# Kernel tuning notes

Hardware: AMD Instinct MI355X
Metric: run time of the kernel (lower is better)

## Reference

```python
import jax, jax.numpy as jnp
import numpy as np

S1, S2 = 1024, 1024
DA, DV, DOUT = 2, 64, 1
K1, K2 = 32, 32


def _gelu(x):
    # torch nn.GELU() default is the exact erf-based gelu
    return jax.nn.gelu(x, approximate=False)


def _flayer(Rr, Ri, w, x):
    f = jnp.fft.rfftn(x, axes=(0, 1))[:K1, :K2]            # [K1,K2,DV] complex
    Rf = jnp.einsum('abc,abcd->abd', f, Rr + 1j * Ri)       # [K1,K2,DV] complex
    kernelpart = jnp.fft.irfftn(Rf, s=(S1, S2), axes=(0, 1))  # [S1,S2,DV] real
    return _gelu(kernelpart + x @ w)


def setup_inputs() -> dict:
    key = jax.random.key(0)
    ks = jax.random.split(key, 20)
    d = {}
    d['input'] = jax.random.normal(ks[0], (S1, S2, DA), dtype=jnp.float32)
    d['Wsh'] = jax.random.normal(ks[1], (DA, DV), dtype=jnp.float32) * (1.0 / np.sqrt(DA))
    d['bsh'] = jax.random.normal(ks[2], (DV,), dtype=jnp.float32) * 0.02
    for i, base in zip(range(1, 5), range(3, 15, 3)):
        d[f'Rr{i}'] = jax.random.normal(ks[base], (K1, K2, DV, DV), dtype=jnp.float32) * (1.0 / DV)
        d[f'Ri{i}'] = jax.random.normal(ks[base + 1], (K1, K2, DV, DV), dtype=jnp.float32) * (1.0 / DV)
        d[f'w{i}'] = jax.random.normal(ks[base + 2], (DV, DV), dtype=jnp.float32) * (1.0 / np.sqrt(DV))
    d['Wp'] = jax.random.normal(ks[15], (DV, DOUT), dtype=jnp.float32) * (1.0 / np.sqrt(DV))
    d['bp'] = jax.random.normal(ks[16], (DOUT,), dtype=jnp.float32) * 0.02
    return d


def reference(input, Wsh, bsh, Rr1, Ri1, w1, Rr2, Ri2, w2,
              Rr3, Ri3, w3, Rr4, Ri4, w4, Wp, bp):
    vt = _gelu(input @ Wsh + bsh)          # Shallow: Linear + GELU
    vt = _flayer(Rr1, Ri1, w1, vt)
    vt = _flayer(Rr2, Ri2, w2, vt)
    vt = _flayer(Rr3, Ri3, w3, vt)
    vt = _flayer(Rr4, Ri4, w4, vt)
    u = (vt @ Wp + bp)[:, :, 0]            # Project, take channel 0 -> [S1,S2]
    return u
```

## Files before the change

### kernel.cpp

```cpp
#include <hip/hip_runtime.h>
#include <math.h>

#define MASKN 1023

typedef unsigned short ushort_t;
typedef __attribute__((ext_vector_type(8))) short short8;
typedef __attribute__((ext_vector_type(4))) float floatx4;
typedef __attribute__((ext_vector_type(4))) unsigned short us4v;

__device__ __forceinline__ float gelu_f(float x) {
    float x2 = x * x;
    float inner = fmaf(0.044715f * x, x2, x);
    float t = exp2f(inner * -2.302089214f);
    return x * __builtin_amdgcn_rcpf(1.0f + t);
}

__device__ __forceinline__ float bf2f(ushort_t h) {
    return __uint_as_float(((unsigned int)h) << 16);
}
__device__ __forceinline__ ushort_t f2bf(float f) {
    unsigned int u = __float_as_uint(f);
    u += 0x7FFFu + ((u >> 16) & 1u);
    return (ushort_t)(u >> 16);
}
struct us4 { ushort_t x, y, z, w; };

__device__ __forceinline__ unsigned int pk2bf(float lo, float hi) {
    unsigned int r;
    asm("v_cvt_pk_bf16_f32 %0, %1, %2" : "=v"(r) : "v"(lo), "v"(hi));
    return r;
}

__device__ __forceinline__ void st4(ushort_t* p, float4 v) {
    uint2 w;
    w.x = pk2bf(v.x, v.y);
    w.y = pk2bf(v.z, v.w);
    *(uint2*)p = w;
}

__device__ __forceinline__ void async16(ushort_t* l, const ushort_t* g) {
    __builtin_amdgcn_global_load_lds(
        (const __attribute__((address_space(1))) void*)g,
        (__attribute__((address_space(3))) void*)l, 16, 0, 0);
}

__global__ void k_fill_tw(float* __restrict__ ct, float* __restrict__ st) {
    int j = blockIdx.x * 256 + threadIdx.x;
    float ang = (float)j * (6.283185307179586f / 1024.0f);
    float s, c;
    sincosf(ang, &s, &c);
    ct[j] = c; st[j] = s;
}

__global__ void k_fill_T1(ushort_t* __restrict__ T1h, ushort_t* __restrict__ T1l) {
    int idx = blockIdx.x * 256 + threadIdx.x;
    int k2p = idx >> 10, y = idx & 1023;
    int k2 = k2p >> 1;
    float ang = (float)((k2 * y) & MASKN) * (6.283185307179586f / 1024.0f);
    float s, c;
    sincosf(ang, &s, &c);
    float v = (k2p & 1) ? -s : c;
    ushort_t h = f2bf(v);
    T1h[idx] = h;
    T1l[idx] = f2bf(v - bf2f(h));
}

__global__ void k_fill_T2(ushort_t* __restrict__ T2h, ushort_t* __restrict__ T2l) {
    int idx = blockIdx.x * 256 + threadIdx.x;
    int n2 = idx >> 6, kk = idx & 63;
    int k2 = kk >> 1;
    float ang = (float)((k2 * n2) & MASKN) * (6.283185307179586f / 1024.0f);
    float s, c;
    sincosf(ang, &s, &c);
    float v = (kk & 1) ? -s : c;
    ushort_t h = f2bf(v);
    T2h[idx] = h;
    T2l[idx] = f2bf(v - bf2f(h));
}

__global__ void k_fill_wT(const float* __restrict__ w1, const float* __restrict__ w2,
        const float* __restrict__ w3, const float* __restrict__ w4,
        ushort_t* __restrict__ wTh, ushort_t* __restrict__ wTl) {
    int l = blockIdx.y;
    int i = blockIdx.x * 256 + threadIdx.x;
    int d = i >> 6, c = i & 63;
    const float* w = (l == 0) ? w1 : (l == 1) ? w2 : (l == 2) ? w3 : w4;
    float v = w[c * 64 + d];
    ushort_t h = f2bf(v);
    wTh[l * 4096 + i] = h;
    wTl[l * 4096 + i] = f2bf(v - bf2f(h));
}

__global__ __launch_bounds__(256) void k_shallow(const float* __restrict__ in,
        const float* __restrict__ Wsh, const float* __restrict__ bsh,
        ushort_t* __restrict__ vt) {
    int tid = blockIdx.x * 256 + threadIdx.x;
    int p = tid >> 4, c0 = (tid & 15) << 2;
    float a0 = in[p * 2], a1 = in[p * 2 + 1];
    float4 w0 = *(const float4*)&Wsh[c0];
    float4 w1 = *(const float4*)&Wsh[64 + c0];
    float4 b  = *(const float4*)&bsh[c0];
    float4 r;
    r.x = gelu_f(fmaf(a0, w0.x, fmaf(a1, w1.x, b.x)));
    r.y = gelu_f(fmaf(a0, w0.y, fmaf(a1, w1.y, b.y)));
    r.z = gelu_f(fmaf(a0, w0.z, fmaf(a1, w1.z, b.z)));
    r.w = gelu_f(fmaf(a0, w0.w, fmaf(a1, w1.w, b.w)));
    st4(&vt[(size_t)p * 64 + c0], r);
}

#define VS1 72
__global__ __launch_bounds__(256, 3) void k_f1(const ushort_t* __restrict__ vt,
        const ushort_t* __restrict__ T1h, const ushort_t* __restrict__ T1l,
        float* __restrict__ gT) {
    __shared__ __align__(16) ushort_t t1s[2][8192];
    __shared__ __align__(16) ushort_t vs[2][64 * VS1];
    int t = threadIdx.x;
    int x0 = blockIdx.x * 2;
    int wv = t >> 6, lane = t & 63;
    int lm = lane & 15, quad = lane >> 4;
    int lrow = t & 63, cq = (t >> 6) * 16;
    const ushort_t* vrow0 = vt + (size_t)x0 * 65536;
    const ushort_t* vrow1 = vrow0 + 65536;

    floatx4 acc[2][4];
    #pragma unroll
    for (int xi = 0; xi < 2; ++xi)
        #pragma unroll
        for (int nt = 0; nt < 4; ++nt) acc[xi][nt] = (floatx4)(0.f);

    uint4 pf[2][2][2];
    #pragma unroll
    for (int i = 0; i < 4; ++i) {
        int j = (wv * 4 + i) * 64 + lane;
        int jj = j & 511;
        int r = jj >> 3, du = jj & 7, su = du ^ (r & 7);
        const ushort_t* src = ((j < 512) ? T1h : T1l) + (size_t)r * 1024 + su * 8;
        async16(&t1s[0][(wv * 4 + i) * 512], src);
    }
    __builtin_amdgcn_sched_barrier(0);
    {
        const ushort_t* s00 = vrow0 + (size_t)lrow * 64 + cq;
        pf[0][0][0] = *(const uint4*)(s00);
        pf[0][0][1] = *(const uint4*)(s00 + 8);
        const ushort_t* s01 = vrow1 + (size_t)lrow * 64 + cq;
        pf[0][1][0] = *(const uint4*)(s01);
        pf[0][1][1] = *(const uint4*)(s01 + 8);
        const ushort_t* s10 = vrow0 + (size_t)(64 + lrow) * 64 + cq;
        pf[1][0][0] = *(const uint4*)(s10);
        pf[1][0][1] = *(const uint4*)(s10 + 8);
        const ushort_t* s11 = vrow1 + (size_t)(64 + lrow) * 64 + cq;
        pf[1][1][0] = *(const uint4*)(s11);
        pf[1][1][1] = *(const uint4*)(s11 + 8);
    }
    __builtin_amdgcn_sched_barrier(0);

    for (int hc = 0; hc < 16; ++hc) {
        int b = hc & 1;
        #pragma unroll
        for (int xi = 0; xi < 2; ++xi)
            #pragma unroll
            for (int i = 0; i < 2; ++i) {
                union { uint4 u; ushort_t e[8]; } uv;
                uv.u = pf[b][xi][i];
                #pragma unroll
                for (int j = 0; j < 8; ++j)
                    vs[xi][(cq + i * 8 + j) * VS1 + lrow] = uv.e[j];
            }
        __builtin_amdgcn_sched_barrier(0);
        if (hc < 15) asm volatile("s_waitcnt vmcnt(4)" ::: "memory");
        else         asm volatile("s_waitcnt vmcnt(0)" ::: "memory");
        __builtin_amdgcn_sched_barrier(0);
        __builtin_amdgcn_s_barrier();
        if (hc < 15) {
            #pragma unroll
            for (int i = 0; i < 4; ++i) {
                int j = (wv * 4 + i) * 64 + lane;
                int jj = j & 511;
                int r = jj >> 3, du = jj & 7, su = du ^ (r & 7);
                const ushort_t* src = ((j < 512) ? T1h : T1l)
                                      + (size_t)r * 1024 + (hc + 1) * 64 + su * 8;
                async16(&t1s[b ^ 1][(wv * 4 + i) * 512], src);
            }
        }
        if (hc < 14) {
            const ushort_t* s0 = vrow0 + (size_t)((hc + 2) * 64 + lrow) * 64 + cq;
            pf[b][0][0] = *(const uint4*)(s0);
            pf[b][0][1] = *(const uint4*)(s0 + 8);
            const ushort_t* s1 = vrow1 + (size_t)((hc + 2) * 64 + lrow) * 64 + cq;
            pf[b][1][0] = *(const uint4*)(s1);
            pf[b][1][1] = *(const uint4*)(s1 + 8);
        }
        __builtin_amdgcn_sched_barrier(0);

        #pragma unroll
        for (int ys = 0; ys < 2; ++ys) {
            short8 af0 = *(const short8*)&vs[0][(wv * 16 + lm) * VS1 + ys * 32 + quad * 8];
            short8 af1 = *(const short8*)&vs[1][(wv * 16 + lm) * VS1 + ys * 32 + quad * 8];
            #pragma unroll
            for (int nt = 0; nt < 4; ++nt) {
                int sl = (((ys * 4 + quad) ^ (lm & 7)) * 8);
                short8 bh = *(const short8*)&t1s[b][(nt * 16 + lm) * 64 + sl];
                short8 bl = *(const short8*)&t1s[b][4096 + (nt * 16 + lm) * 64 + sl];
                acc[0][nt] = __builtin_amdgcn_mfma_f32_16x16x32_bf16(af0, bh, acc[0][nt], 0, 0, 0);
                acc[0][nt] = __builtin_amdgcn_mfma_f32_16x16x32_bf16(af0, bl, acc[0][nt], 0, 0, 0);
                acc[1][nt] = __builtin_amdgcn_mfma_f32_16x16x32_bf16(af1, bh, acc[1][nt], 0, 0, 0);
                acc[1][nt] = __builtin_amdgcn_mfma_f32_16x16x32_bf16(af1, bl, acc[1][nt], 0, 0, 0);
            }
        }
    }
    #pragma unroll
    for (int xi = 0; xi < 2; ++xi) {
        float* grow = gT + (size_t)(x0 + xi) * 4096;
        #pragma unroll
        for (int nt = 0; nt < 4; ++nt)
            #pragma unroll
            for (int r = 0; r < 4; ++r)
                grow[(wv * 16 + quad * 4 + r) * 64 + nt * 16 + lm] = acc[xi][nt][r];
    }
}

__global__ __launch_bounds__(256) void k_f2(const float* __restrict__ gT,
        const float* __restrict__ ct, const float* __restrict__ st,
        float* __restrict__ fpr, float* __restrict__ fpi) {
    int t = threadIdx.x;
    int cx = blockIdx.x;
    int cg = blockIdx.y;
    int k10 = blockIdx.z * 8;
    int l = t & 63;
    int q = t >> 6;
    int c = cg * 4 + q;
    int e = l & 1;
    int k2 = l >> 1;
    float acc[8];
    #pragma unroll
    for (int i = 0; i < 8; ++i) acc[i] = 0.f;
    for (int xi = 0; xi < 128; ++xi) {
        int x = cx * 128 + xi;
        float v = gT[(size_t)x * 4096 + c * 64 + l];
        float p = __shfl_xor(v, 1);
        float gr = e ? p : v;
        float gi = e ? v : p;
        float u  = e ? gi : gr;
        float w2 = e ? -gr : gi;
        float cb = ct[x], sb = st[x];
        int ph = (x * k10) & MASKN;
        float cr = ct[ph], sr = st[ph];
        #pragma unroll
        for (int j = 0; j < 8; ++j) {
            acc[j] = fmaf(u, cr, fmaf(w2, sr, acc[j]));
            float nc = fmaf(cr, cb, -sr * sb);
            float ns = fmaf(sr, cb, cr * sb);
            cr = nc; sr = ns;
        }
    }
    float* dst = e ? fpi : fpr;
    #pragma unroll
    for (int j = 0; j < 8; ++j)
        dst[(size_t)cx * 65536 + ((k10 + j) * 32 + k2) * 64 + c] = acc[j];
}

__global__ __launch_bounds__(64) void k_mix(const float* __restrict__ fpr, const float* __restrict__ fpi,
        const float* __restrict__ Rr, const float* __restrict__ Ri,
        float* __restrict__ Rfr, float* __restrict__ Rfi) {
    __shared__ float fr[64], fi[64];
    int m = blockIdx.x;
    int d = threadIdx.x;
    float sr = 0.f, si = 0.f;
    #pragma unroll
    for (int ch = 0; ch < 8; ++ch) {
        sr += fpr[(size_t)ch * 65536 + m * 64 + d];
        si += fpi[(size_t)ch * 65536 + m * 64 + d];
    }
    fr[d] = sr; fi[d] = si;
    __syncthreads();
    const float* Rrb = Rr + (size_t)m * 4096;
    const float* Rib = Ri + (size_t)m * 4096;
    float ar = 0.f, ai = 0.f;
    for (int c = 0; c < 64; ++c) {
        float rr = Rrb[c * 64 + d], ri = Rib[c * 64 + d];
        ar = fmaf(fr[c], rr, fmaf(-fi[c], ri, ar));
        ai = fmaf(fr[c], ri, fmaf(fi[c], rr, ai));
    }
    Rfr[m * 64 + d] = ar;
    Rfi[m * 64 + d] = ai;
}

__global__ __launch_bounds__(256) void k_i1(const float* __restrict__ Rfr, const float* __restrict__ Rfi,
        const float* __restrict__ ctg, const float* __restrict__ stg,
        ushort_t* __restrict__ Bhl) {
    __shared__ float ct[1024], st[1024];
    int t = threadIdx.x;
    #pragma unroll
    for (int i = 0; i < 4; ++i) { int j = t + 256 * i; ct[j] = ctg[j]; st[j] = stg[j]; }
    __syncthreads();
    int n1 = blockIdx.x;
    int d = t & 63;
    int k20 = (t >> 6) * 8;
    float br[8], bi[8];
    #pragma unroll
    for (int j = 0; j < 8; ++j) { br[j] = 0.f; bi[j] = 0.f; }
    int idx = 0;
    for (int k1 = 0; k1 < 32; ++k1) {
        float cc = ct[idx], ss = st[idx];
        idx = (idx + n1) & MASKN;
        #pragma unroll
        for (int j = 0; j < 8; ++j) {
            float rr = Rfr[(k1 * 32 + k20 + j) * 64 + d];
            float ri = Rfi[(k1 * 32 + k20 + j) * 64 + d];
            br[j] = fmaf(rr, cc, fmaf(-ri, ss, br[j]));
            bi[j] = fmaf(rr, ss, fmaf(ri, cc, bi[j]));
        }
    }
    union { uint4 u[2]; ushort_t e[16]; } hh, ll;
    #pragma unroll
    for (int j = 0; j < 8; ++j) {
        int k2 = k20 + j;
        float sc = (k2 == 0 ? 1.0f : 2.0f) * 9.5367431640625e-7f;
        float vr = br[j] * sc, vi = bi[j] * sc;
        ushort_t hr = f2bf(vr), hi2 = f2bf(vi);
        hh.e[2 * j] = hr;          hh.e[2 * j + 1] = hi2;
        ll.e[2 * j] = f2bf(vr - bf2f(hr));
        ll.e[2 * j + 1] = f2bf(vi - bf2f(hi2));
    }
    size_t base = (size_t)n1 * 8192 + d * 64 + 2 * k20;
    *(uint4*)(Bhl + base) = hh.u[0];
    *(uint4*)(Bhl + base + 8) = hh.u[1];
    *(uint4*)(Bhl + 4096 + base) = ll.u[0];
    *(uint4*)(Bhl + 4096 + base + 8) = ll.u[1];
}

__global__ __launch_bounds__(256, 2) void k_i2f(ushort_t* __restrict__ vt,
        ushort_t* Bhl,
        const ushort_t* __restrict__ T2h, const ushort_t* __restrict__ T2l,
        const ushort_t* __restrict__ wTh, const ushort_t* __restrict__ wTl,
        const ushort_t* __restrict__ T1h, const ushort_t* __restrict__ T1l,
        float* gT) {
    __shared__ __align__(16) ushort_t ab[16384];
    __shared__ __align__(16) ushort_t t1s[2][8192];
    __shared__ __align__(16) ushort_t trans[2][4096];
    int t = threadIdx.x;
    int wv = t >> 6, lane = t & 63;
    int lm = lane & 15, quad = lane >> 4;
    int n1 = blockIdx.x;
    const ushort_t* Bhr = Bhl + (size_t)n1 * 8192;
    const ushort_t* Blr = Bhr + 4096;

    {
        const ushort_t* s = (wv == 0) ? Bhr : (wv == 1) ? Blr : (wv == 2) ? wTh : wTl;
        #pragma unroll
        for (int i = 0; i < 8; ++i) {
            int j = i * 64 + lane;
            int r = j >> 3, u = (j & 7) ^ (r & 7);
            async16(&ab[wv * 4096 + i * 512], s + r * 64 + u * 8);
        }
    }
    #pragma unroll
    for (int i = 0; i < 4; ++i) {
        int j = (wv * 4 + i) * 64 + lane;
        int jj = j & 511;
        int rr_ = jj >> 3, du = jj & 7, su = du ^ (rr_ & 7);
        const ushort_t* src = ((j < 512) ? T1h : T1l) + (size_t)rr_ * 1024 + su * 8;
        async16(&t1s[0][(wv * 4 + i) * 512], src);
    }

    int n2b = wv * 16 + lm;
    const ushort_t* t2hp = T2h + n2b * 64 + quad * 8;
    const ushort_t* t2lp = T2l + n2b * 64 + quad * 8;
    const ushort_t* vrd  = vt + ((size_t)n1 * 1024 + n2b) * 64 + quad * 8;
    ushort_t*       vst  = vt + ((size_t)n1 * 1024 + n2b) * 64;

    short8 th[2][2], tl[2][2], vv[2][2];
    #pragma unroll
    for (int ks = 0; ks < 2; ++ks) {
        th[0][ks] = *(const short8*)(t2hp + ks * 32);
        tl[0][ks] = *(const short8*)(t2lp + ks * 32);
        vv[0][ks] = *(const short8*)(vrd + ks * 32);
    }
    floatx4 facc[4];
    #pragma unroll
    for (int nt = 0; nt < 4; ++nt) facc[nt] = (floatx4)(0.f);
    __syncthreads();

    int r7 = lm & 7;
    int u3 = n2b >> 3, e3 = n2b & 7;
    #pragma unroll
    for (int c = 0; c < 16; ++c) {
        int b = c & 1;
        {
            #pragma unroll
            for (int ks = 0; ks < 2; ++ks) {
                th[b ^ 1][ks] = *(const short8*)(t2hp + (c + 1) * 4096 + ks * 32);
                tl[b ^ 1][ks] = *(const short8*)(t2lp + (c + 1) * 4096 + ks * 32);
                vv[b ^ 1][ks] = *(const short8*)(vrd + (size_t)(c + 1) * 4096 + ks * 32);
            }
        }
        __builtin_amdgcn_sched_barrier(0);

        floatx4 acc[4];
        #pragma unroll
        for (int mt = 0; mt < 4; ++mt) acc[mt] = (floatx4)(0.f);
        __builtin_amdgcn_s_setprio(1);
        #pragma unroll
        for (int ks = 0; ks < 2; ++ks) {
            int sl = ((ks * 4 + quad) ^ r7) * 8;
            #pragma unroll
            for (int mt = 0; mt < 4; ++mt) {
                int ro = (mt * 16 + lm) * 64 + sl;
                short8 ah = *(const short8*)&ab[ro];
                short8 al = *(const short8*)&ab[4096 + ro];
                short8 wh = *(const short8*)&ab[8192 + ro];
                short8 wl = *(const short8*)&ab[12288 + ro];
                acc[mt] = __builtin_amdgcn_mfma_f32_16x16x32_bf16(ah, th[b][ks], acc[mt], 0, 0, 0);
                acc[mt] = __builtin_amdgcn_mfma_f32_16x16x32_bf16(al, th[b][ks], acc[mt], 0, 0, 0);
                acc[mt] = __builtin_amdgcn_mfma_f32_16x16x32_bf16(ah, tl[b][ks], acc[mt], 0, 0, 0);
                acc[mt] = __builtin_amdgcn_mfma_f32_16x16x32_bf16(wh, vv[b][ks], acc[mt], 0, 0, 0);
                acc[mt] = __builtin_amdgcn_mfma_f32_16x16x32_bf16(wl, vv[b][ks], acc[mt], 0, 0, 0);
            }
        }
        __builtin_amdgcn_s_setprio(0);

        uint2 w[4];
        #pragma unroll
        for (int mt = 0; mt < 4; ++mt) {
            w[mt].x = pk2bf(gelu_f(acc[mt][0]), gelu_f(acc[mt][1]));
            w[mt].y = pk2bf(gelu_f(acc[mt][2]), gelu_f(acc[mt][3]));
            *(uint2*)(vst + (size_t)c * 4096 + mt * 16 + quad * 4) = w[mt];
        }
        ushort_t* tb = trans[b];
        #pragma unroll
        for (int mt = 0; mt < 4; ++mt) {
            int chb = mt * 16 + quad * 4;
            #pragma unroll
            for (int r = 0; r < 4; ++r) {
                int ch = chb + r;
                ushort_t val = (r == 0) ? (ushort_t)(w[mt].x & 0xffffu)
                             : (r == 1) ? (ushort_t)(w[mt].x >> 16)
                             : (r == 2) ? (ushort_t)(w[mt].y & 0xffffu)
                                        : (ushort_t)(w[mt].y >> 16);
                tb[ch * 64 + ((u3 ^ (ch & 7)) << 3) + e3] = val;
            }
        }
        __builtin_amdgcn_sched_barrier(0);
        asm volatile("s_waitcnt lgkmcnt(0)" ::: "memory");
        asm volatile("s_waitcnt vmcnt(10)" ::: "memory");
        __builtin_amdgcn_sched_barrier(0);
        __builtin_amdgcn_s_barrier();
        __builtin_amdgcn_sched_barrier(0);

        #pragma unroll
        for (int i = 0; i < 4; ++i) {
            int j = (wv * 4 + i) * 64 + lane;
            int jj = j & 511;
            int rr_ = jj >> 3, du = jj & 7, su = du ^ (rr_ & 7);
            const ushort_t* src = ((j < 512) ? T1h : T1l)
                                  + (size_t)rr_ * 1024 + (c + 1) * 64 + su * 8;
            async16(&t1s[b ^ 1][(wv * 4 + i) * 512], src);
        }
        __builtin_amdgcn_sched_barrier(0);

        #pragma unroll
        for (int ys = 0; ys < 2; ++ys) {
            int ch = wv * 16 + lm;
            short8 af = *(const short8*)&trans[b][ch * 64 + (((ys * 4 + quad) ^ (ch & 7)) << 3)];
            #pragma unroll
            for (int nt = 0; nt < 4; ++nt) {
                int sl = ((ys * 4 + quad) ^ r7) * 8;
                short8 bh = *(const short8*)&t1s[b][(nt * 16 + lm) * 64 + sl];
                short8 bl = *(const short8*)&t1s[b][4096 + (nt * 16 + lm) * 64 + sl];
                facc[nt] = __builtin_amdgcn_mfma_f32_16x16x32_bf16(af, bh, facc[nt], 0, 0, 0);
                facc[nt] = __builtin_amdgcn_mfma_f32_16x16x32_bf16(af, bl, facc[nt], 0, 0, 0);
            }
        }
        __builtin_amdgcn_sched_barrier(0);
    }

    float* grow = gT + (size_t)n1 * 4096;
    #pragma unroll
    for (int nt = 0; nt < 4; ++nt)
        #pragma unroll
        for (int r = 0; r < 4; ++r)
            grow[(wv * 16 + quad * 4 + r) * 64 + nt * 16 + lm] = facc[nt][r];
}

__global__ __launch_bounds__(256, 4) void k_i2fin(ushort_t* __restrict__ vt,
        const ushort_t* __restrict__ Bhl,
        const ushort_t* __restrict__ T2h, const ushort_t* __restrict__ T2l,
        const ushort_t* __restrict__ wTh, const ushort_t* __restrict__ wTl,
        const float* __restrict__ Wp, const float* __restrict__ bp,
        float* __restrict__ out) {
    __shared__ __align__(16) ushort_t ab[16384];
    int t = threadIdx.x;
    int wv = t >> 6, lane = t & 63;
    int lm = lane & 15, quad = lane >> 4;
    int n1 = blockIdx.x;
    const ushort_t* Bhr = Bhl + (size_t)n1 * 8192;
    const ushort_t* Blr = Bhr + 4096;
    {
        const ushort_t* s = (wv == 0) ? Bhr : (wv == 1) ? Blr : (wv == 2) ? wTh : wTl;
        #pragma unroll
        for (int i = 0; i < 8; ++i) {
            int j = i * 64 + lane;
            int r = j >> 3, u = (j & 7) ^ (r & 7);
            async16(&ab[wv * 4096 + i * 512], s + r * 64 + u * 8);
        }
    }
    int n2b = wv * 16 + lm;
    const ushort_t* t2hp = T2h + n2b * 64 + quad * 8;
    const ushort_t* t2lp = T2l + n2b * 64 + quad * 8;
    const ushort_t* vrd  = vt + ((size_t)n1 * 1024 + n2b) * 64 + quad * 8;
    short8 th[2][2], tl[2][2], vv[2][2];
    #pragma unroll
    for (int ks = 0; ks < 2; ++ks) {
        th[0][ks] = *(const short8*)(t2hp + ks * 32);
        tl[0][ks] = *(const short8*)(t2lp + ks * 32);
        vv[0][ks] = *(const short8*)(vrd + ks * 32);
    }
    float4 wpv[4];
    float bp0 = bp[0];
    #pragma unroll
    for (int mt = 0; mt < 4; ++mt) wpv[mt] = *(const float4*)&Wp[mt * 16 + quad * 4];
    __syncthreads();

    int r7 = lm & 7;
    #pragma unroll
    for (int c = 0; c < 16; ++c) {
        if (c < 15) {
            #pragma unroll
            for (int ks = 0; ks < 2; ++ks) {
                th[(c + 1) & 1][ks] = *(const short8*)(t2hp + (c + 1) * 4096 + ks * 32);
                tl[(c + 1) & 1][ks] = *(const short8*)(t2lp + (c + 1) * 4096 + ks * 32);
                vv[(c + 1) & 1][ks] = *(const short8*)(vrd + (size_t)(c + 1) * 4096 + ks * 32);
            }
        }
        __builtin_amdgcn_sched_barrier(0);
        floatx4 acc[4];
        #pragma unroll
        for (int mt = 0; mt < 4; ++mt) acc[mt] = (floatx4)(0.f);
        __builtin_amdgcn_s_setprio(1);
        #pragma unroll
        for (int ks = 0; ks < 2; ++ks) {
            int sl = ((ks * 4 + quad) ^ r7) * 8;
            #pragma unroll
            for (int mt = 0; mt < 4; ++mt) {
                int ro = (mt * 16 + lm) * 64 + sl;
                short8 ah = *(const short8*)&ab[ro];
                short8 al = *(const short8*)&ab[4096 + ro];
                short8 wh = *(const short8*)&ab[8192 + ro];
                short8 wl = *(const short8*)&ab[12288 + ro];
                acc[mt] = __builtin_amdgcn_mfma_f32_16x16x32_bf16(ah, th[c & 1][ks], acc[mt], 0, 0, 0);
                acc[mt] = __builtin_amdgcn_mfma_f32_16x16x32_bf16(al, th[c & 1][ks], acc[mt], 0, 0, 0);
                acc[mt] = __builtin_amdgcn_mfma_f32_16x16x32_bf16(ah, tl[c & 1][ks], acc[mt], 0, 0, 0);
                acc[mt] = __builtin_amdgcn_mfma_f32_16x16x32_bf16(wh, vv[c & 1][ks], acc[mt], 0, 0, 0);
                acc[mt] = __builtin_amdgcn_mfma_f32_16x16x32_bf16(wl, vv[c & 1][ks], acc[mt], 0, 0, 0);
            }
        }
        __builtin_amdgcn_s_setprio(0);
        float s = 0.f;
        #pragma unroll
        for (int mt = 0; mt < 4; ++mt) {
            s = fmaf(gelu_f(acc[mt][0]), wpv[mt].x, s);
            s = fmaf(gelu_f(acc[mt][1]), wpv[mt].y, s);
            s = fmaf(gelu_f(acc[mt][2]), wpv[mt].z, s);
            s = fmaf(gelu_f(acc[mt][3]), wpv[mt].w, s);
        }
        s += __shfl_xor(s, 16);
        s += __shfl_xor(s, 32);
        if (quad == 0)
            out[(size_t)n1 * 1024 + c * 64 + n2b] = s + bp0;
    }
}

extern "C" void kernel_launch(void* const* d_in, const int* in_sizes, int n_in,
                              void* d_out, int out_size, void* d_ws, size_t ws_size,
                              hipStream_t stream) {
    const float* in  = (const float*)d_in[0];
    const float* Wsh = (const float*)d_in[1];
    const float* bsh = (const float*)d_in[2];
    const float* Wp  = (const float*)d_in[15];
    const float* bp  = (const float*)d_in[16];

    char* wsb = (char*)d_ws;
    ushort_t* vt   = (ushort_t*)wsb;
    float* ctab = (float*)(wsb + 134217728);
    float* stab = ctab + 1024;
    float* gT   = stab + 1024;
    float* Rfr  = gT + 4194304;
    float* Rfi  = Rfr + 65536;
    ushort_t* T1h = (ushort_t*)(Rfi + 65536);
    ushort_t* T1l = T1h + 65536;
    ushort_t* T2h = T1l + 65536;
    ushort_t* T2l = T2h + 65536;
    ushort_t* wTh = T2l + 65536;
    ushort_t* wTl = wTh + 16384;
    ushort_t* Bhl = (ushort_t*)gT;
    float* fpr = (float*)d_out;
    float* fpi = fpr + 524288;

    k_fill_tw<<<4, 256, 0, stream>>>(ctab, stab);
    k_fill_T1<<<256, 256, 0, stream>>>(T1h, T1l);
    k_fill_T2<<<256, 256, 0, stream>>>(T2h, T2l);
    k_fill_wT<<<dim3(16, 4), 256, 0, stream>>>((const float*)d_in[5], (const float*)d_in[8],
                                               (const float*)d_in[11], (const float*)d_in[14], wTh, wTl);
    k_shallow<<<65536, 256, 0, stream>>>(in, Wsh, bsh, vt);
    k_f1<<<512, 256, 0, stream>>>(vt, T1h, T1l, gT);
    for (int L = 0; L < 4; ++L) {
        const float* Rr = (const float*)d_in[3 + L * 3];
        const float* Ri = (const float*)d_in[4 + L * 3];
        k_f2<<<dim3(8, 16, 4), 256, 0, stream>>>(gT, ctab, stab, fpr, fpi);
        k_mix<<<1024, 64, 0, stream>>>(fpr, fpi, Rr, Ri, Rfr, Rfi);
        k_i1<<<1024, 256, 0, stream>>>(Rfr, Rfi, ctab, stab, Bhl);
        if (L < 3) {
            k_i2f<<<1024, 256, 0, stream>>>(vt, Bhl, T2h, T2l,
                    wTh + L * 4096, wTl + L * 4096, T1h, T1l, gT);
        } else {
            k_i2fin<<<1024, 256, 0, stream>>>(vt, Bhl, T2h, T2l,
                    wTh + L * 4096, wTl + L * 4096, Wp, bp, (float*)d_out);
        }
    }
}
```

Before: 716.7 us.

## Stage GELU output through LDS for coalesced stores and single-buffer T1/trans tiles

The per-chunk GELU output is first written into a padded LDS tile (vtile), then copied out as 16-byte coalesced rows instead of scattered 8-byte per-lane global stores. To make room in LDS, the t1s and trans buffers go from double to single buffering. The T1 async load now happens at the start of each iteration rather than one iteration ahead, and a second barrier per iteration is added. This trades load-ahead overlap and extra synchronisation for better write coalescing and possibly lower LDS use.

```diff
diff --git a/kernel.cpp b/kernel.cpp
--- a/kernel.cpp
+++ b/kernel.cpp
@@ -336,8 +336,9 @@
         const ushort_t* __restrict__ T1h, const ushort_t* __restrict__ T1l,
         float* gT) {
     __shared__ __align__(16) ushort_t ab[16384];
-    __shared__ __align__(16) ushort_t t1s[2][8192];
-    __shared__ __align__(16) ushort_t trans[2][4096];
+    __shared__ __align__(16) ushort_t t1s[8192];
+    __shared__ __align__(16) ushort_t trans[4096];
+    __shared__ __align__(16) ushort_t vtile[64 * VS1];
     int t = threadIdx.x;
     int wv = t >> 6, lane = t & 63;
     int lm = lane & 15, quad = lane >> 4;
@@ -354,20 +355,12 @@
             async16(&ab[wv * 4096 + i * 512], s + r * 64 + u * 8);
         }
     }
-    #pragma unroll
-    for (int i = 0; i < 4; ++i) {
-        int j = (wv * 4 + i) * 64 + lane;
-        int jj = j & 511;
-        int rr_ = jj >> 3, du = jj & 7, su = du ^ (rr_ & 7);
-        const ushort_t* src = ((j < 512) ? T1h : T1l) + (size_t)rr_ * 1024 + su * 8;
-        async16(&t1s[0][(wv * 4 + i) * 512], src);
-    }
 
     int n2b = wv * 16 + lm;
     const ushort_t* t2hp = T2h + n2b * 64 + quad * 8;
     const ushort_t* t2lp = T2l + n2b * 64 + quad * 8;
     const ushort_t* vrd  = vt + ((size_t)n1 * 1024 + n2b) * 64 + quad * 8;
-    ushort_t*       vst  = vt + ((size_t)n1 * 1024 + n2b) * 64;
+    ushort_t*       vstw = vt + ((size_t)n1 * 1024 + wv * 16) * 64;
 
     short8 th[2][2], tl[2][2], vv[2][2];
     #pragma unroll
@@ -383,16 +376,26 @@
 
     int r7 = lm & 7;
     int u3 = n2b >> 3, e3 = n2b & 7;
+    int srow = lane >> 2;
+    int scol = (lane & 3) * 8;
     #pragma unroll
     for (int c = 0; c < 16; ++c) {
         int b = c & 1;
-        {
-            #pragma unroll
-            for (int ks = 0; ks < 2; ++ks) {
-                th[b ^ 1][ks] = *(const short8*)(t2hp + (c + 1) * 4096 + ks * 32);
-                tl[b ^ 1][ks] = *(const short8*)(t2lp + (c + 1) * 4096 + ks * 32);
-                vv[b ^ 1][ks] = *(const short8*)(vrd + (size_t)(c + 1) * 4096 + ks * 32);
-            }
+        #pragma unroll
+        for (int i = 0; i < 4; ++i) {
+            int j = (wv * 4 + i) * 64 + lane;
+            int jj = j & 511;
+            int rr_ = jj >> 3, du = jj & 7, su = du ^ (rr_ & 7);
+            const ushort_t* src = ((j < 512) ? T1h : T1l)
+                                  + (size_t)rr_ * 1024 + c * 64 + su * 8;
+            async16(&t1s[(wv * 4 + i) * 512], src);
+        }
+        __builtin_amdgcn_sched_barrier(0);
+        #pragma unroll
+        for (int ks = 0; ks < 2; ++ks) {
+            th[b ^ 1][ks] = *(const short8*)(t2hp + (c + 1) * 4096 + ks * 32);
+            tl[b ^ 1][ks] = *(const short8*)(t2lp + (c + 1) * 4096 + ks * 32);
+            vv[b ^ 1][ks] = *(const short8*)(vrd + (size_t)(c + 1) * 4096 + ks * 32);
         }
         __builtin_amdgcn_sched_barrier(0);
 
@@ -424,9 +427,8 @@
         for (int mt = 0; mt < 4; ++mt) {
             w[mt].x = pk2bf(gelu_f(acc[mt][0]), gelu_f(acc[mt][1]));
             w[mt].y = pk2bf(gelu_f(acc[mt][2]), gelu_f(acc[mt][3]));
-            *(uint2*)(vst + (size_t)c * 4096 + mt * 16 + quad * 4) = w[mt];
-        }
-        ushort_t* tb = trans[b];
+            *(uint2*)&vtile[n2b * VS1 + mt * 16 + quad * 4] = w[mt];
+        }
         #pragma unroll
         for (int mt = 0; mt < 4; ++mt) {
             int chb = mt * 16 + quad * 4;
@@ -437,40 +439,38 @@
                              : (r == 1) ? (ushort_t)(w[mt].x >> 16)
                              : (r == 2) ? (ushort_t)(w[mt].y & 0xffffu)
                                         : (ushort_t)(w[mt].y >> 16);
-                tb[ch * 64 + ((u3 ^ (ch & 7)) << 3) + e3] = val;
+                trans[ch * 64 + ((u3 ^ (ch & 7)) << 3) + e3] = val;
             }
         }
         __builtin_amdgcn_sched_barrier(0);
         asm volatile("s_waitcnt lgkmcnt(0)" ::: "memory");
-        asm volatile("s_waitcnt vmcnt(10)" ::: "memory");
+        asm volatile("s_waitcnt vmcnt(6)" ::: "memory");
         __builtin_amdgcn_sched_barrier(0);
         __builtin_amdgcn_s_barrier();
         __builtin_amdgcn_sched_barrier(0);
 
         #pragma unroll
-        for (int i = 0; i < 4; ++i) {
-            int j = (wv * 4 + i) * 64 + lane;
-            int jj = j & 511;
-            int rr_ = jj >> 3, du = jj & 7, su = du ^ (rr_ & 7);
-            const ushort_t* src = ((j < 512) ? T1h : T1l)
-                                  + (size_t)rr_ * 1024 + (c + 1) * 64 + su * 8;
-            async16(&t1s[b ^ 1][(wv * 4 + i) * 512], src);
+        for (int s = 0; s < 2; ++s) {
+            uint4 d4 = *(const uint4*)&vtile[(wv * 16 + srow) * VS1 + scol + s * 32];
+            *(uint4*)(vstw + (size_t)c * 4096 + srow * 64 + scol + s * 32) = d4;
         }
         __builtin_amdgcn_sched_barrier(0);
 
         #pragma unroll
         for (int ys = 0; ys < 2; ++ys) {
             int ch = wv * 16 + lm;
-            short8 af = *(const short8*)&trans[b][ch * 64 + (((ys * 4 + quad) ^ (ch & 7)) << 3)];
+            short8 af = *(const short8*)&trans[ch * 64 + (((ys * 4 + quad) ^ (ch & 7)) << 3)];
             #pragma unroll
             for (int nt = 0; nt < 4; ++nt) {
                 int sl = ((ys * 4 + quad) ^ r7) * 8;
-                short8 bh = *(const short8*)&t1s[b][(nt * 16 + lm) * 64 + sl];
-                short8 bl = *(const short8*)&t1s[b][4096 + (nt * 16 + lm) * 64 + sl];
+                short8 bh = *(const short8*)&t1s[(nt * 16 + lm) * 64 + sl];
+                short8 bl = *(const short8*)&t1s[4096 + (nt * 16 + lm) * 64 + sl];
                 facc[nt] = __builtin_amdgcn_mfma_f32_16x16x32_bf16(af, bh, facc[nt], 0, 0, 0);
                 facc[nt] = __builtin_amdgcn_mfma_f32_16x16x32_bf16(af, bl, facc[nt], 0, 0, 0);
             }
         }
+        __builtin_amdgcn_sched_barrier(0);
+        __builtin_amdgcn_s_barrier();
         __builtin_amdgcn_sched_barrier(0);
     }
 
```

Result: no change. 721.0 us (+0.6%).
